# Performance work log

Measured on AMD Instinct MI355X. Metric: run time of the kernel, lower is better.

The kernel has to match this reference:

```python
import jax, jax.numpy as jnp
import numpy as np

H = 16            # num heads
D_NOPE = 128
D_ROPE = 64
D_V = 128
Q_LORA = 1536
KV_LORA = 512
HIDDEN = 2048
EPS = 1e-6


def rmsnorm(x, w):
    xf = x.astype(jnp.float32)
    var = jnp.mean(xf * xf, axis=-1, keepdims=True)
    return (w * (xf * jax.lax.rsqrt(var + EPS))).astype(x.dtype)


def rope_interleaved(x, cos, sin):
    # x: [B,H,S,D]; cos,sin: [S,D] -> use even-index entries as the per-pair values
    B, nH, S, D = x.shape
    cv = cos[:, 0::2].astype(jnp.float32)[None, None]  # [1,1,S,D/2]
    sv = sin[:, 0::2].astype(jnp.float32)[None, None]
    xf = x.astype(jnp.float32).reshape(B, nH, S, D // 2, 2)
    xr, xi = xf[..., 0], xf[..., 1]
    out = jnp.stack([xr * cv - xi * sv, xr * sv + xi * cv], axis=-1)
    return out.reshape(B, nH, S, D).astype(x.dtype)


def setup_inputs() -> dict:
    key = jax.random.key(0)
    ks = jax.random.split(key, 9)
    B, S = 2, 2048
    std = 0.02
    return {
        "hidden_states": jax.random.normal(ks[0], (B, S, HIDDEN), jnp.float32),
        "cos": jax.random.uniform(ks[1], (S, D_ROPE), jnp.float32),
        "sin": jax.random.uniform(ks[2], (S, D_ROPE), jnp.float32),
        "q_a_w": jax.random.normal(ks[3], (HIDDEN, Q_LORA), jnp.float32) * std,
        "q_a_ln_w": jnp.ones((Q_LORA,), jnp.float32),
        "q_b_w": jax.random.normal(ks[4], (Q_LORA, H * (D_NOPE + D_ROPE)), jnp.float32) * std,
        "kv_a_w": jax.random.normal(ks[5], (HIDDEN, KV_LORA + D_ROPE), jnp.float32) * std,
        "kv_a_ln_w": jnp.ones((KV_LORA,), jnp.float32),
        "kv_b_w": jax.random.normal(ks[6], (KV_LORA, H * (D_NOPE + D_V)), jnp.float32) * std,
        "o_w": jax.random.normal(ks[7], (H * D_V, HIDDEN), jnp.float32) * std,
    }


def reference(hidden_states, cos, sin, q_a_w, q_a_ln_w, q_b_w, kv_a_w, kv_a_ln_w, kv_b_w, o_w):
    B, S, _ = hidden_states.shape
    scale = 1.0 / np.sqrt(D_NOPE + D_ROPE)

    # Q path: low-rank down-proj, RMSNorm, up-proj
    q = rmsnorm(hidden_states @ q_a_w, q_a_ln_w) @ q_b_w
    q = q.reshape(B, S, H, D_NOPE + D_ROPE).transpose(0, 2, 1, 3)  # [B,H,S,Dq]
    q_nope, q_rope = q[..., :D_NOPE], q[..., D_NOPE:]

    # KV path: compressed kv + shared rope key
    ckv = hidden_states @ kv_a_w  # [B,S,KV_LORA+D_ROPE]
    compressed_kv, k_rope = ckv[..., :KV_LORA], ckv[..., KV_LORA:]
    k_rope = jnp.broadcast_to(k_rope[:, None], (B, H, S, D_ROPE))
    kv = rmsnorm(compressed_kv, kv_a_ln_w) @ kv_b_w
    kv = kv.reshape(B, S, H, D_NOPE + D_V).transpose(0, 2, 1, 3)  # [B,H,S,Dk+Dv]
    k_nope, value = kv[..., :D_NOPE], kv[..., D_NOPE:]

    q_rope = rope_interleaved(q_rope, cos, sin)
    k_rope = rope_interleaved(k_rope, cos, sin)

    query = jnp.concatenate([q_nope, q_rope], axis=-1)  # [B,H,S,192]
    key = jnp.concatenate([k_nope, k_rope], axis=-1)

    attn = jnp.einsum("bhqd,bhkd->bhqk", query, key) * scale
    attn = jax.nn.softmax(attn.astype(jnp.float32), axis=-1).astype(query.dtype)
    out = jnp.einsum("bhqk,bhkd->bhqd", attn, value)  # [B,H,S,Dv]
    out = out.transpose(0, 2, 1, 3).reshape(B, S, H * D_V)
    return out @ o_w
```

## Files before the change

### kernel.cpp

```cpp
#include <hip/hip_runtime.h>

typedef unsigned short u16;
typedef __bf16 bf16x8 __attribute__((ext_vector_type(8)));
typedef float f32x4 __attribute__((ext_vector_type(4)));
typedef u16 u16x4 __attribute__((ext_vector_type(4)));

#define S_ 2048

__device__ __forceinline__ u16 f2bf(float f) {
  union { float f; unsigned u; } v; v.f = f;
  unsigned r = v.u + 0x7fffu + ((v.u >> 16) & 1u);
  return (u16)(r >> 16);
}

__device__ __forceinline__ f32x4 mfma16(bf16x8 a, bf16x8 b, f32x4 c) {
  return __builtin_amdgcn_mfma_f32_16x16x32_bf16(a, b, c, 0, 0, 0);
}

__device__ __forceinline__ void async16(const void* g, void* l) {
  __builtin_amdgcn_global_load_lds((__attribute__((address_space(1))) void*)g,
                                   (__attribute__((address_space(3))) void*)l,
                                   16, 0, 0);
}

#define QSCALE2 0.10411756755f

__global__ __launch_bounds__(256)
void prep_k(const float* __restrict__ hs, u16* __restrict__ hs_bf,
            const float* __restrict__ q_a_w, const float* __restrict__ kv_a_w,
            const float* __restrict__ q_b_w, const float* __restrict__ kv_b_w,
            const float* __restrict__ o_w,
            u16* __restrict__ qakvT, u16* __restrict__ qbwT,
            u16* __restrict__ kvbwT, u16* __restrict__ owT) {
  int blk = blockIdx.x;
  int tid = threadIdx.x;
  if (blk < 4096) {
    int i = blk * 256 + tid;
    f32x4 a = ((const f32x4*)hs)[2 * i], b = ((const f32x4*)hs)[2 * i + 1];
    union { u16 v[8]; f32x4 q; } u;
#pragma unroll
    for (int e = 0; e < 4; ++e) { u.v[e] = f2bf(a[e]); u.v[4 + e] = f2bf(b[e]); }
    ((f32x4*)hs_bf)[i] = u.q;
    return;
  }
  blk -= 4096;
  const float* W; u16* Wt; int K, N, gx;
  if (blk < 3072)       { W = q_a_w;  Wt = qakvT;                     K = 2048; N = 1536; gx = 64; }
  else if (blk < 4352)  { blk -= 3072;  W = kv_a_w; Wt = qakvT + (long)1536 * 2048; K = 2048; N = 576;  gx = 64; }
  else if (blk < 8960)  { blk -= 4352;  W = q_b_w;  Wt = qbwT;  K = 1536; N = 3072; gx = 48; }
  else if (blk < 11008) { blk -= 8960;  W = kv_b_w; Wt = kvbwT; K = 512;  N = 4096; gx = 16; }
  else                  { blk -= 11008; W = o_w;    Wt = owT;   K = 2048; N = 2048; gx = 64; }
  int k0 = (blk % gx) * 32, n0 = (blk / gx) * 32;
  int tx = tid & 31, ty = tid >> 5;
  __shared__ float tile[32][33];
#pragma unroll
  for (int r = 0; r < 32; r += 8) {
    int n = n0 + tx;
    tile[ty + r][tx] = (n < N) ? W[(long)(k0 + ty + r) * N + n] : 0.f;
  }
  __syncthreads();
#pragma unroll
  for (int r = 0; r < 32; r += 8) {
    Wt[(long)(n0 + ty + r) * K + k0 + tx] = f2bf(tile[tx][ty + r]);
  }
}

__device__ __forceinline__ int xcd_chunk(int lin, int nwg) {
  if ((nwg & 7) == 0) return (lin & 7) * (nwg >> 3) + (lin >> 3);
  return lin;
}

template <typename OUT_T, bool ROPE>
__global__ __launch_bounds__(256)
void gemm_bt_k(const u16* __restrict__ A, const u16* __restrict__ Bt,
               OUT_T* __restrict__ C, int K, int Nc, int ldc,
               const float* __restrict__ cs, const float* __restrict__ sn) {
  __shared__ __align__(16) u16 sA[2][128 * 32];
  __shared__ __align__(16) u16 sB[2][128 * 32];
  int tid = threadIdx.x;
  int lane = tid & 63, w = tid >> 6;
  int wr = w >> 1, wc = w & 1;
  int l15 = lane & 15, quad = lane >> 4;
  int gx = gridDim.x;
  int nl = xcd_chunk(blockIdx.x + gx * blockIdx.y, gx * gridDim.y);
  long tm = (long)(nl / gx) * 128;
  long tn = (long)(nl % gx) * 128;
  const u16* Ab = A + tm * K;
  const u16* Bb = Bt + tn * K;
  f32x4 acc[4][4] = {};

#pragma unroll
  for (int it = 0; it < 2; ++it) {
    int c = tid + it * 256;
    int row = c >> 2, sl = c & 3;
    int kc = sl ^ ((row >> 1) & 3);
    async16(Ab + (long)row * K + kc * 8, &sA[0][c * 8]);
    async16(Bb + (long)row * K + kc * 8, &sB[0][c * 8]);
  }

  int nk = K >> 5;
  for (int kt = 0; kt < nk; ++kt) {
    int cur = kt & 1;
    __syncthreads();
    if (kt + 1 < nk) {
      int k0n = (kt + 1) << 5;
#pragma unroll
      for (int it = 0; it < 2; ++it) {
        int c = tid + it * 256;
        int row = c >> 2, sl = c & 3;
        int kc = sl ^ ((row >> 1) & 3);
        async16(Ab + (long)row * K + k0n + kc * 8, &sA[cur ^ 1][c * 8]);
        async16(Bb + (long)row * K + k0n + kc * 8, &sB[cur ^ 1][c * 8]);
      }
    }
    bf16x8 af[4], bfr[4];
#pragma unroll
    for (int i = 0; i < 4; ++i) {
      int rowa = wr * 64 + i * 16 + l15;
      int slot = quad ^ ((rowa >> 1) & 3);
      af[i] = *(const bf16x8*)(&sA[cur][(rowa * 4 + slot) * 8]);
    }
#pragma unroll
    for (int j = 0; j < 4; ++j) {
      int rowb = wc * 64 + j * 16 + l15;
      int slot = quad ^ ((rowb >> 1) & 3);
      bfr[j] = *(const bf16x8*)(&sB[cur][(rowb * 4 + slot) * 8]);
    }
#pragma unroll
    for (int i = 0; i < 4; ++i)
#pragma unroll
      for (int j = 0; j < 4; ++j)
        acc[i][j] = mfma16(af[i], bfr[j], acc[i][j]);
  }
#pragma unroll
  for (int i = 0; i < 4; ++i) {
#pragma unroll
    for (int j = 0; j < 4; ++j) {
      int col = (int)tn + wc * 64 + j * 16 + l15;
      if (col < Nc) {
        bool ropeT = false;
        int fi = 0;
        if constexpr (ROPE) {
          int d = col % 192;
          ropeT = (d >= 128);
          fi = (d - 128) & ~1;
        }
#pragma unroll
        for (int r = 0; r < 4; ++r) {
          long row = tm + wr * 64 + i * 16 + quad * 4 + r;
          float v = acc[i][j][r];
          if constexpr (ROPE) {
            float partner = __shfl_xor(v, 1);
            if (ropeT) {
              int si = (int)row & (S_ - 1);
              float cv = cs[si * 64 + fi], sv = sn[si * 64 + fi];
              v = (l15 & 1) ? (partner * sv + v * cv)
                            : (v * cv - partner * sv);
            }
            v *= QSCALE2;
          }
          if constexpr (sizeof(OUT_T) == 2) C[row * ldc + col] = f2bf(v);
          else                              C[row * ldc + col] = v;
        }
      }
    }
  }
}

__global__ __launch_bounds__(256)
void gemm_kvb_k(const u16* __restrict__ A, const u16* __restrict__ Bt,
                u16* __restrict__ kswz, u16* __restrict__ vswz,
                const u16* __restrict__ kr) {
  const int K = 512;
  __shared__ __align__(16) u16 sA[2][128 * 32];
  __shared__ __align__(16) u16 sB[2][128 * 32];
  int tid = threadIdx.x;
  int lane = tid & 63, w = tid >> 6;
  int wr = w >> 1, wc = w & 1;
  int l15 = lane & 15, quad = lane >> 4;
  int gx = gridDim.x;
  int nl = xcd_chunk(blockIdx.x + gx * blockIdx.y, gx * gridDim.y);
  long tm = (long)(nl / gx) * 128;
  long tn = (long)(nl % gx) * 128;
  const u16* Ab = A + tm * K;
  const u16* Bb = Bt + tn * K;
  f32x4 acc[4][4] = {};

#pragma unroll
  for (int it = 0; it < 2; ++it) {
    int c = tid + it * 256;
    int row = c >> 2, sl = c & 3;
    int kc = sl ^ ((row >> 1) & 3);
    async16(Ab + (long)row * K + kc * 8, &sA[0][c * 8]);
    async16(Bb + (long)row * K + kc * 8, &sB[0][c * 8]);
  }

  const int nk = K >> 5;
  for (int kt = 0; kt < nk; ++kt) {
    int cur = kt & 1;
    __syncthreads();
    if (kt + 1 < nk) {
      int k0n = (kt + 1) << 5;
#pragma unroll
      for (int it = 0; it < 2; ++it) {
        int c = tid + it * 256;
        int row = c >> 2, sl = c & 3;
        int kc = sl ^ ((row >> 1) & 3);
        async16(Ab + (long)row * K + k0n + kc * 8, &sA[cur ^ 1][c * 8]);
        async16(Bb + (long)row * K + k0n + kc * 8, &sB[cur ^ 1][c * 8]);
      }
    }
    bf16x8 af[4], bfr[4];
#pragma unroll
    for (int i = 0; i < 4; ++i) {
      int rowa = wr * 64 + i * 16 + l15;
      int slot = quad ^ ((rowa >> 1) & 3);
      af[i] = *(const bf16x8*)(&sA[cur][(rowa * 4 + slot) * 8]);
    }
#pragma unroll
    for (int j = 0; j < 4; ++j) {
      int rowb = wc * 64 + j * 16 + l15;
      int slot = quad ^ ((rowb >> 1) & 3);
      bfr[j] = *(const bf16x8*)(&sB[cur][(rowb * 4 + slot) * 8]);
    }
#pragma unroll
    for (int i = 0; i < 4; ++i)
#pragma unroll
      for (int j = 0; j < 4; ++j)
        acc[i][j] = mfma16(af[i], bfr[j], acc[i][j]);
  }

  int h = (int)(tn >> 8);
  int b = (int)(tm >> 11);
  int kt0 = ((int)tm & 2047) >> 6;
  int tile = (b * 16 + h) * 32 + kt0 + wr;
  if ((tn & 255) == 0) {
    u16* dst = kswz + (long)tile * 12288;
#pragma unroll
    for (int i = 0; i < 4; ++i) {
#pragma unroll
      for (int j = 0; j < 4; ++j) {
        int frag = quad * 6 + wc * 2 + (j >> 1);
        int chunk = frag * 64 + ((j & 1) * 2 + (l15 >> 3)) * 16 + i * 4;
#pragma unroll
        for (int r = 0; r < 4; ++r)
          dst[(chunk + r) * 8 + (l15 & 7)] = f2bf(acc[i][j][r]);
      }
    }
#pragma unroll
    for (int it = 0; it < 4; ++it) {
      int c = tid + it * 256;
      int tt = c >> 9;
      int cc = c & 511;
      int lane2 = cc & 63, fd = cc >> 6;
      int kg = fd >> 1, dbr = fd & 1;
      int sl = lane2 & 15;
      int key = (kt0 + tt) * 64 + (sl >> 2) * 16 + kg * 4 + (sl & 3);
      int doff = dbr * 32 + (lane2 >> 4) * 8;
      int frag = kg * 6 + 4 + dbr;
      u16* dst2 = kswz + (long)((b * 16 + h) * 32 + kt0 + tt) * 12288;
      *(f32x4*)(dst2 + (frag * 64 + lane2) * 8) =
          *(const f32x4*)(kr + ((long)(b * S_ + key)) * 64 + doff);
    }
  } else {
    u16* dst = vswz + (long)tile * 8192;
    int kq = quad >> 1;
    int e0 = (quad & 1) * 4;
#pragma unroll
    for (int i = 0; i < 4; ++i) {
#pragma unroll
      for (int j = 0; j < 4; ++j) {
        int frag = kq * 8 + wc * 4 + j;
        u16x4 pk;
#pragma unroll
        for (int r = 0; r < 4; ++r) pk[r] = f2bf(acc[i][j][r]);
        *(u16x4*)(dst + (frag * 64 + i * 16 + l15) * 8 + e0) = pk;
      }
    }
  }
}

__global__ __launch_bounds__(256)
void rmsnorm2_k(const float* __restrict__ qsrc, int ldq,
                const float* __restrict__ kvsrc, int ldkv,
                const float* __restrict__ wq, const float* __restrict__ wkv,
                u16* __restrict__ qout, u16* __restrict__ kvout,
                const float* __restrict__ cs, const float* __restrict__ sn,
                u16* __restrict__ krout) {
  int blk = blockIdx.x;
  if (blk >= 8192) {
    int idx = (blk - 8192) * 256 + threadIdx.x;
    int row = idx >> 5, i = idx & 31;
    int s = row & (S_ - 1);
    const float* src = qsrc + 2048;
    float xr = src[(long)row * ldq + 2 * i];
    float xi = src[(long)row * ldq + 2 * i + 1];
    float cv = cs[s * 64 + 2 * i], sv = sn[s * 64 + 2 * i];
    krout[(long)row * 64 + 2 * i]     = f2bf(xr * cv - xi * sv);
    krout[(long)row * 64 + 2 * i + 1] = f2bf(xr * sv + xi * cv);
    return;
  }
  const float* x; const float* wt; u16* o; int N;
  if (blk < 4096) { x = qsrc + (long)blk * ldq;  wt = wq;  o = qout + (long)blk * 1536;  N = 1536; }
  else { blk -= 4096; x = kvsrc + (long)blk * ldkv; wt = wkv; o = kvout + (long)blk * 512; N = 512; }
  float ss = 0.f;
  for (int i = threadIdx.x; i < N; i += 256) { float v = x[i]; ss += v * v; }
#pragma unroll
  for (int off = 32; off; off >>= 1) ss += __shfl_down(ss, off);
  __shared__ float red[4];
  if ((threadIdx.x & 63) == 0) red[threadIdx.x >> 6] = ss;
  __syncthreads();
  float inv = rsqrtf((red[0] + red[1] + red[2] + red[3]) / N + 1e-6f);
  for (int i = threadIdx.x; i < N; i += 256) o[i] = f2bf(wt[i] * x[i] * inv);
}

__global__ __launch_bounds__(256, 2)
void attn_k(const u16* __restrict__ qb, const u16* __restrict__ kswz,
            const u16* __restrict__ vswz, u16* __restrict__ attnO) {
  int lin = blockIdx.x + 16 * blockIdx.y;
  int xcd = lin & 7;
  int j = lin >> 3;
  int bh = (xcd << 2) + (j >> 4);
  int qt = j & 15;
  int b = bh >> 4, h = bh & 15;
  int tid = threadIdx.x, lane = tid & 63, w = tid >> 6;
  int l15 = lane & 15, quad = lane >> 4;
  int qrow0 = qt * 128 + w * 32;

  __shared__ __align__(16) u16 sK[2][24 * 64 * 8];
  __shared__ __align__(16) u16 sV[2][16 * 64 * 8];

  const u16* Kb = kswz + (long)bh * 32 * 12288;
  const u16* Vb = vswz + (long)bh * 32 * 8192;

  bf16x8 qf[2][6];
#pragma unroll
  for (int rg = 0; rg < 2; ++rg) {
    const u16* qp = qb + ((long)(b * S_ + qrow0 + rg * 16 + l15)) * 3072 + h * 192 + quad * 8;
#pragma unroll
    for (int kb = 0; kb < 6; ++kb) qf[rg][kb] = *(const bf16x8*)(qp + kb * 32);
  }

  union { u16 v[8]; bf16x8 b; } ones;
#pragma unroll
  for (int e = 0; e < 8; ++e) ones.v[e] = 0x3F80;

  f32x4 o[2][8] = {};
  f32x4 lacc[2] = {};

#pragma unroll
  for (int i = 0; i < 6; ++i) { int c = tid + i * 256; async16(Kb + c * 8, &sK[0][c * 8]); }
#pragma unroll
  for (int i = 0; i < 4; ++i) { int c = tid + i * 256; async16(Vb + c * 8, &sV[0][c * 8]); }

#pragma unroll 1
  for (int kt = 0; kt < 32; ++kt) {
    int cur = kt & 1;
    __syncthreads();
    if (kt < 31) {
      const u16* Kt = Kb + (long)(kt + 1) * 12288;
      const u16* Vt = Vb + (long)(kt + 1) * 8192;
#pragma unroll
      for (int i = 0; i < 6; ++i) { int c = tid + i * 256; async16(Kt + c * 8, &sK[cur ^ 1][c * 8]); }
#pragma unroll
      for (int i = 0; i < 4; ++i) { int c = tid + i * 256; async16(Vt + c * 8, &sV[cur ^ 1][c * 8]); }
    }

    const u16* kbase = sK[cur];
    const u16* vbase = sV[cur];

    f32x4 s[2][4] = {};
    __builtin_amdgcn_s_setprio(1);
#pragma unroll
    for (int kg = 0; kg < 4; ++kg) {
#pragma unroll
      for (int db = 0; db < 6; ++db) {
        bf16x8 kf = *(const bf16x8*)(kbase + ((kg * 6 + db) * 64 + lane) * 8);
        s[0][kg] = mfma16(kf, qf[0][db], s[0][kg]);
        s[1][kg] = mfma16(kf, qf[1][db], s[1][kg]);
      }
    }
    __builtin_amdgcn_s_setprio(0);

    bf16x8 pf[2][2];
#pragma unroll
    for (int rg = 0; rg < 2; ++rg) {
#pragma unroll
      for (int kg = 0; kg < 4; ++kg) {
#pragma unroll
        for (int r = 0; r < 4; ++r)
          s[rg][kg][r] = __builtin_amdgcn_exp2f(s[rg][kg][r]);
      }
#pragma unroll
      for (int kq = 0; kq < 2; ++kq) {
        union { unsigned wd[4]; bf16x8 v; } u;
        asm("v_cvt_pk_bf16_f32 %0, %1, %2"
            : "=v"(u.wd[0]) : "v"(s[rg][2 * kq][0]), "v"(s[rg][2 * kq][1]));
        asm("v_cvt_pk_bf16_f32 %0, %1, %2"
            : "=v"(u.wd[1]) : "v"(s[rg][2 * kq][2]), "v"(s[rg][2 * kq][3]));
        asm("v_cvt_pk_bf16_f32 %0, %1, %2"
            : "=v"(u.wd[2]) : "v"(s[rg][2 * kq + 1][0]), "v"(s[rg][2 * kq + 1][1]));
        asm("v_cvt_pk_bf16_f32 %0, %1, %2"
            : "=v"(u.wd[3]) : "v"(s[rg][2 * kq + 1][2]), "v"(s[rg][2 * kq + 1][3]));
        pf[rg][kq] = u.v;
      }
      lacc[rg] = mfma16(pf[rg][0], ones.b, lacc[rg]);
      lacc[rg] = mfma16(pf[rg][1], ones.b, lacc[rg]);
    }

    __builtin_amdgcn_s_setprio(1);
#pragma unroll
    for (int kq = 0; kq < 2; ++kq) {
#pragma unroll
      for (int j2 = 0; j2 < 8; ++j2) {
        bf16x8 vf = *(const bf16x8*)(vbase + ((kq * 8 + j2) * 64 + lane) * 8);
        o[0][j2] = mfma16(pf[0][kq], vf, o[0][j2]);
        o[1][j2] = mfma16(pf[1][kq], vf, o[1][j2]);
      }
    }
    __builtin_amdgcn_s_setprio(0);
  }

#pragma unroll
  for (int rg = 0; rg < 2; ++rg) {
    u16* op = attnO + ((long)(b * S_ + qrow0 + rg * 16)) * 2048 + h * 128;
    float invr[4];
#pragma unroll
    for (int r = 0; r < 4; ++r) invr[r] = 1.f / lacc[rg][r];
#pragma unroll
    for (int j2 = 0; j2 < 8; ++j2)
#pragma unroll
      for (int r = 0; r < 4; ++r)
        op[(long)(quad * 4 + r) * 2048 + j2 * 16 + l15] = f2bf(o[rg][j2][r] * invr[r]);
  }
}

extern "C" void kernel_launch(void* const* d_in, const int* in_sizes, int n_in,
                              void* d_out, int out_size, void* d_ws, size_t ws_size,
                              hipStream_t stream) {
  const float* hs      = (const float*)d_in[0];
  const float* cosb    = (const float*)d_in[1];
  const float* sinb    = (const float*)d_in[2];
  const float* q_a_w   = (const float*)d_in[3];
  const float* q_a_ln  = (const float*)d_in[4];
  const float* q_b_w   = (const float*)d_in[5];
  const float* kv_a_w  = (const float*)d_in[6];
  const float* kv_a_ln = (const float*)d_in[7];
  const float* kv_b_w  = (const float*)d_in[8];
  const float* o_w     = (const float*)d_in[9];
  float* out = (float*)d_out;
  (void)in_sizes; (void)n_in; (void)out_size; (void)ws_size;

  char* p = (char*)d_ws;
  auto alloc = [&](size_t b) { char* r = p; p += (b + 255) & ~((size_t)255); return r; };
  u16*   hs_bf  = (u16*)  alloc((size_t)4096 * 2048 * 2);
  u16*   qakvT  = (u16*)  alloc((size_t)2176 * 2048 * 2);
  u16*   qbwT   = (u16*)  alloc((size_t)3072 * 1536 * 2);
  u16*   kvbwT  = (u16*)  alloc((size_t)4096 * 512  * 2);
  u16*   owT    = (u16*)  alloc((size_t)2048 * 2048 * 2);
  float* qa_ckv = (float*)alloc((size_t)4096 * 2176 * 4);
  u16*   qan    = (u16*)  alloc((size_t)4096 * 1536 * 2);
  u16*   ckvn   = (u16*)  alloc((size_t)4096 * 512  * 2);
  u16*   kr     = (u16*)  alloc((size_t)4096 * 64   * 2);
  u16*   qbuf   = (u16*)  alloc((size_t)4096 * 3072 * 2);
  u16*   aO     = (u16*)  alloc((size_t)4096 * 2048 * 2);
  u16* kswz = (u16*)qa_ckv;
  u16* vswz = (u16*)hs_bf;

  prep_k<<<19200, 256, 0, stream>>>(hs, hs_bf, q_a_w, kv_a_w, q_b_w, kv_b_w,
                                    o_w, qakvT, qbwT, kvbwT, owT);

  gemm_bt_k<float, false><<<dim3(17, 32), 256, 0, stream>>>(
      hs_bf, qakvT, qa_ckv, 2048, 2176, 2176, nullptr, nullptr);
  rmsnorm2_k<<<8704, 256, 0, stream>>>(qa_ckv, 2176, qa_ckv + 1536, 2176,
                                       q_a_ln, kv_a_ln, qan, ckvn,
                                       cosb, sinb, kr);
  gemm_bt_k<u16, true><<<dim3(24, 32), 256, 0, stream>>>(
      qan, qbwT, qbuf, 1536, 3072, 3072, cosb, sinb);
  gemm_kvb_k<<<dim3(32, 32), 256, 0, stream>>>(ckvn, kvbwT, kswz, vswz, kr);
  attn_k<<<dim3(16, 32), 256, 0, stream>>>(qbuf, kswz, vswz, aO);
  gemm_bt_k<float, false><<<dim3(16, 32), 256, 0, stream>>>(
      aO, owT, out, 2048, 2048, 2048, nullptr, nullptr);
}
```

Measured before the change: 460.8 us.

## Double GEMM K-tile depth and load attention V directly into registers

```diff
diff --git a/kernel.cpp b/kernel.cpp
--- a/kernel.cpp
+++ b/kernel.cpp
@@ -75,8 +75,8 @@
 void gemm_bt_k(const u16* __restrict__ A, const u16* __restrict__ Bt,
                OUT_T* __restrict__ C, int K, int Nc, int ldc,
                const float* __restrict__ cs, const float* __restrict__ sn) {
-  __shared__ __align__(16) u16 sA[2][128 * 32];
-  __shared__ __align__(16) u16 sB[2][128 * 32];
+  __shared__ __align__(16) u16 sA[2][128 * 64];
+  __shared__ __align__(16) u16 sB[2][128 * 64];
   int tid = threadIdx.x;
   int lane = tid & 63, w = tid >> 6;
   int wr = w >> 1, wc = w & 1;
@@ -90,47 +90,50 @@
   f32x4 acc[4][4] = {};
 
 #pragma unroll
-  for (int it = 0; it < 2; ++it) {
+  for (int it = 0; it < 4; ++it) {
     int c = tid + it * 256;
-    int row = c >> 2, sl = c & 3;
-    int kc = sl ^ ((row >> 1) & 3);
+    int row = c >> 3, sl = c & 7;
+    int kc = sl ^ (row & 7);
     async16(Ab + (long)row * K + kc * 8, &sA[0][c * 8]);
     async16(Bb + (long)row * K + kc * 8, &sB[0][c * 8]);
   }
 
-  int nk = K >> 5;
+  int nk = K >> 6;
   for (int kt = 0; kt < nk; ++kt) {
     int cur = kt & 1;
     __syncthreads();
     if (kt + 1 < nk) {
-      int k0n = (kt + 1) << 5;
-#pragma unroll
-      for (int it = 0; it < 2; ++it) {
+      int k0n = (kt + 1) << 6;
+#pragma unroll
+      for (int it = 0; it < 4; ++it) {
         int c = tid + it * 256;
-        int row = c >> 2, sl = c & 3;
-        int kc = sl ^ ((row >> 1) & 3);
-        async16(Ab + (long)row * K + k0n + kc * 8, &sA[cur ^ 1][c * 8]);
-        async16(Bb + (long)row * K + k0n + kc * 8, &sB[cur ^ 1][c * 8]);
-      }
-    }
-    bf16x8 af[4], bfr[4];
-#pragma unroll
-    for (int i = 0; i < 4; ++i) {
-      int rowa = wr * 64 + i * 16 + l15;
-      int slot = quad ^ ((rowa >> 1) & 3);
-      af[i] = *(const bf16x8*)(&sA[cur][(rowa * 4 + slot) * 8]);
-    }
-#pragma unroll
-    for (int j = 0; j < 4; ++j) {
-      int rowb = wc * 64 + j * 16 + l15;
-      int slot = quad ^ ((rowb >> 1) & 3);
-      bfr[j] = *(const bf16x8*)(&sB[cur][(rowb * 4 + slot) * 8]);
-    }
-#pragma unroll
-    for (int i = 0; i < 4; ++i)
-#pragma unroll
-      for (int j = 0; j < 4; ++j)
-        acc[i][j] = mfma16(af[i], bfr[j], acc[i][j]);
+        int row = c >> 3, sl = c & 7;
+        int kc = k0n + ((sl ^ (row & 7)) << 3);
+        async16(Ab + (long)row * K + kc, &sA[cur ^ 1][c * 8]);
+        async16(Bb + (long)row * K + kc, &sB[cur ^ 1][c * 8]);
+      }
+    }
+#pragma unroll
+    for (int ks = 0; ks < 2; ++ks) {
+      bf16x8 af[4], bfr[4];
+#pragma unroll
+      for (int i = 0; i < 4; ++i) {
+        int rowa = wr * 64 + i * 16 + l15;
+        int slot = (ks * 4 + quad) ^ (rowa & 7);
+        af[i] = *(const bf16x8*)(&sA[cur][rowa * 64 + slot * 8]);
+      }
+#pragma unroll
+      for (int j = 0; j < 4; ++j) {
+        int rowb = wc * 64 + j * 16 + l15;
+        int slot = (ks * 4 + quad) ^ (rowb & 7);
+        bfr[j] = *(const bf16x8*)(&sB[cur][rowb * 64 + slot * 8]);
+      }
+#pragma unroll
+      for (int i = 0; i < 4; ++i)
+#pragma unroll
+        for (int j = 0; j < 4; ++j)
+          acc[i][j] = mfma16(af[i], bfr[j], acc[i][j]);
+    }
   }
 #pragma unroll
   for (int i = 0; i < 4; ++i) {
@@ -328,7 +331,6 @@
   int qrow0 = qt * 128 + w * 32;
 
   __shared__ __align__(16) u16 sK[2][24 * 64 * 8];
-  __shared__ __align__(16) u16 sV[2][16 * 64 * 8];
 
   const u16* Kb = kswz + (long)bh * 32 * 12288;
   const u16* Vb = vswz + (long)bh * 32 * 8192;
@@ -350,8 +352,6 @@
 
 #pragma unroll
   for (int i = 0; i < 6; ++i) { int c = tid + i * 256; async16(Kb + c * 8, &sK[0][c * 8]); }
-#pragma unroll
-  for (int i = 0; i < 4; ++i) { int c = tid + i * 256; async16(Vb + c * 8, &sV[0][c * 8]); }
 
 #pragma unroll 1
   for (int kt = 0; kt < 32; ++kt) {
@@ -359,15 +359,17 @@
     __syncthreads();
     if (kt < 31) {
       const u16* Kt = Kb + (long)(kt + 1) * 12288;
-      const u16* Vt = Vb + (long)(kt + 1) * 8192;
 #pragma unroll
       for (int i = 0; i < 6; ++i) { int c = tid + i * 256; async16(Kt + c * 8, &sK[cur ^ 1][c * 8]); }
-#pragma unroll
-      for (int i = 0; i < 4; ++i) { int c = tid + i * 256; async16(Vt + c * 8, &sV[cur ^ 1][c * 8]); }
     }
 
     const u16* kbase = sK[cur];
-    const u16* vbase = sV[cur];
+    const u16* Vt = Vb + (long)kt * 8192;
+
+    bf16x8 vf0[8], vf1[8];
+#pragma unroll
+    for (int f = 0; f < 8; ++f)
+      vf0[f] = *(const bf16x8*)(Vt + (f * 64 + lane) * 8);
 
     f32x4 s[2][4] = {};
     __builtin_amdgcn_s_setprio(1);
@@ -381,6 +383,10 @@
       }
     }
     __builtin_amdgcn_s_setprio(0);
+
+#pragma unroll
+    for (int f = 0; f < 8; ++f)
+      vf1[f] = *(const bf16x8*)(Vt + ((8 + f) * 64 + lane) * 8);
 
     bf16x8 pf[2][2];
 #pragma unroll
@@ -410,13 +416,14 @@
 
     __builtin_amdgcn_s_setprio(1);
 #pragma unroll
-    for (int kq = 0; kq < 2; ++kq) {
-#pragma unroll
-      for (int j2 = 0; j2 < 8; ++j2) {
-        bf16x8 vf = *(const bf16x8*)(vbase + ((kq * 8 + j2) * 64 + lane) * 8);
-        o[0][j2] = mfma16(pf[0][kq], vf, o[0][j2]);
-        o[1][j2] = mfma16(pf[1][kq], vf, o[1][j2]);
-      }
+    for (int j2 = 0; j2 < 8; ++j2) {
+      o[0][j2] = mfma16(pf[0][0], vf0[j2], o[0][j2]);
+      o[1][j2] = mfma16(pf[1][0], vf0[j2], o[1][j2]);
+    }
+#pragma unroll
+    for (int j2 = 0; j2 < 8; ++j2) {
+      o[0][j2] = mfma16(pf[0][1], vf1[j2], o[0][j2]);
+      o[1][j2] = mfma16(pf[1][1], vf1[j2], o[1][j2]);
     }
     __builtin_amdgcn_s_setprio(0);
   }
```

Result: slower. 475.8 us (+3.3%).
